# Kernel tuning notes

Measured on AMD Instinct MI355X. Metric: run time of the kernel, lower is better.

## Reference

```python
import jax, jax.numpy as jnp
import numpy as np

KS = 7                 # sconv_kernel_size
PAD = (KS - 1) // 2
SIMS_SCALE = 10.0      # sims_norm_scale
EPS = 1e-5


def setup_inputs() -> dict:
    key = jax.random.key(0)
    k1, k2, k3, k4 = jax.random.split(key, 4)
    T, C, H, W = 4, 3, 192, 192
    S = 300
    x = jax.random.normal(k1, (T, C, H, W), jnp.float32)
    spix = jax.random.randint(k2, (T, H, W), 0, S, dtype=jnp.int32)
    W_lin = jax.random.normal(k3, (C, C * KS * KS), jnp.float32) * 0.05
    b_lin = jax.random.normal(k4, (C,), jnp.float32) * 0.05
    return {"x": x, "spix": spix, "W_lin": W_lin, "b_lin": b_lin, "n_spix": S}


def _get_sims(x, spix, n_spix, scale):
    # x: [T,C,H,W], spix: [T,H,W] with contiguous ids in [0, n_spix)
    T, C, H, W = x.shape
    feats = x.transpose(0, 2, 3, 1).reshape(T, H * W, C)   # t (h w) f
    ids = spix.reshape(T, H * W)

    def pool(f, i):
        s = jax.ops.segment_sum(f, i, num_segments=n_spix)                      # [S,C]
        c = jax.ops.segment_sum(jnp.ones((f.shape[0],), f.dtype), i, num_segments=n_spix)  # [S]
        return s / jnp.maximum(c, 1.0)[:, None], c

    means, cnt = jax.vmap(pool)(feats, ids)                # [T,S,C], [T,S]
    # squared euclidean distance (cdist ** 2)
    d2 = (jnp.sum(feats * feats, -1)[:, :, None]
          + jnp.sum(means * means, -1)[:, None, :]
          - 2.0 * jnp.einsum('tnc,tsc->tns', feats, means))
    d2 = jnp.maximum(d2, 0.0)                              # [T,HW,S]
    # superpixels absent from frame t get distance inf (pwd[mask] = inf)
    d2 = jnp.where((cnt > 0)[:, None, :], d2, jnp.inf)
    sims = jax.nn.softmax(-scale * d2, axis=-1)            # softmax over superpixels
    return sims.reshape(T, H, W, n_spix)                   # [T,H,W,S]


def _prod_attn(sims):
    # non-local 'prod' search, zero flow, ws=KS: dot product of sims vectors
    # between each pixel and its KSxKS neighborhood (zero-padded borders)
    T, H, W, S = sims.shape
    p = jnp.pad(sims, ((0, 0), (PAD, PAD), (PAD, PAD), (0, 0)))
    attn = [jnp.einsum('thws,thws->thw', sims, p[:, dy:dy + H, dx:dx + W, :])
            for dy in range(KS) for dx in range(KS)]
    return jnp.stack(attn, -1)                             # [T,H,W,KS*KS]


def _unfold(x):
    # torch.nn.Unfold(kernel_size=KS, padding=PAD): zero pad, row-major window
    T, C, H, W = x.shape
    p = jnp.pad(x, ((0, 0), (0, 0), (PAD, PAD), (PAD, PAD)))
    pats = [p[:, :, dy:dy + H, dx:dx + W] for dy in range(KS) for dx in range(KS)]
    return jnp.stack(pats, 2)                              # [T,C,KS*KS,H,W]


def reference(x, spix, W_lin, b_lin, n_spix):
    T, C, H, W = x.shape
    sims = _get_sims(x, spix, n_spix, SIMS_SCALE)          # [T,H,W,S]
    rw = _prod_attn(sims)                                  # [T,H,W,K2]
    # apply_norm('max'): divide by max over neighborhood
    rw = rw / (EPS + jnp.max(rw, axis=-1, keepdims=True))
    Wk = W_lin.reshape(W_lin.shape[0], C, KS * KS)         # [od,id,k2]
    pats = _unfold(x)                                      # [T,id,k2,H,W]
    # out[t,o,h,w] = sum_{i,k} W[o,i,k] * rw[t,h,w,k] * patch[t,i,k,h,w] + b[o]
    out = jnp.einsum('oik,thwk,tikhw->tohw', Wk, rw, pats) + b_lin[None, :, None, None]
    return out
```

## Files before the change

kernel.cpp:

```cpp
#include <hip/hip_runtime.h>
#include <math.h>

#define TT 4
#define HH 192
#define WW 192
#define SS 300
#define SP 320
#define HW (HH*WW)
#define PD 3
#define HSZ 22
#define NHP 484
#define PSTRG 486
#define LOG2E 1.44269504088896340736f
#define NSEG 72
#define MEANS 360448
#define MOFF 393216
#define ZOFF (MOFF + TT*HW)

typedef _Float16 h8 __attribute__((ext_vector_type(8)));
typedef float f4 __attribute__((ext_vector_type(4)));


__launch_bounds__(256)
__global__ void k_accum(const float* __restrict__ x, const int* __restrict__ spix,
                        float* __restrict__ ws) {
    __shared__ float ls[SS * 4];
    const int tid = threadIdx.x;
    const int t = blockIdx.y, seg = blockIdx.x;
    for (int i = tid; i < SS * 4; i += 256) ls[i] = 0.f;
    __syncthreads();
    const int pb = seg * 512 + tid * 2;
#pragma unroll
    for (int it = 0; it < 2; it++) {
        int s = spix[t * HW + pb + it];
        atomicAdd(&ls[s * 4 + 0], x[(t * 3 + 0) * HW + pb + it]);
        atomicAdd(&ls[s * 4 + 1], x[(t * 3 + 1) * HW + pb + it]);
        atomicAdd(&ls[s * 4 + 2], x[(t * 3 + 2) * HW + pb + it]);
        atomicAdd(&ls[s * 4 + 3], 1.f);
    }
    __syncthreads();
    float* part = ws + (t * NSEG + seg) * 1200;
    for (int i = tid; i < SS * 4; i += 256) part[i] = ls[i];
}

__launch_bounds__(256)
__global__ void k_prep(const float* __restrict__ x, float* __restrict__ ws) {
    __shared__ float4 sm[SP];
    const int tid = threadIdx.x;
    const int t = blockIdx.y;
    const float* part = ws + t * NSEG * 1200;
    for (int i = tid; i < SP; i += 256) {
        float4 m;
        if (i < SS) {
            float s0 = 0.f, s1 = 0.f, s2 = 0.f, c = 0.f;
            for (int g = 0; g < NSEG; g++) {
                s0 += part[g * 1200 + i * 4 + 0];
                s1 += part[g * 1200 + i * 4 + 1];
                s2 += part[g * 1200 + i * 4 + 2];
                c  += part[g * 1200 + i * 4 + 3];
            }
            float inv = 1.f / fmaxf(c, 1.f);
            float mx = s0 * inv, my = s1 * inv, mz = s2 * inv;
            m.x = 20.f * LOG2E * mx; m.y = 20.f * LOG2E * my; m.z = 20.f * LOG2E * mz;
            m.w = (c > 0.f) ? (-10.f * LOG2E * (mx * mx + my * my + mz * mz)) : -INFINITY;
        } else {
            m.x = 0.f; m.y = 0.f; m.z = 0.f; m.w = -INFINITY;
        }
        sm[i] = m;
        if (blockIdx.x == 0) ((float4*)(ws + MEANS))[t * SP + i] = m;
    }
    __syncthreads();

    const int p0 = blockIdx.x * 512 + tid;
    const int p1 = p0 + 256;
    const float f0x = x[(t * 3 + 0) * HW + p0], f0y = x[(t * 3 + 1) * HW + p0], f0z = x[(t * 3 + 2) * HW + p0];
    const float f1x = x[(t * 3 + 0) * HW + p1], f1y = x[(t * 3 + 1) * HW + p1], f1z = x[(t * 3 + 2) * HW + p1];

    float M0 = -INFINITY, M1 = -INFINITY;
#pragma unroll 4
    for (int s = 0; s < SS; s++) {
        float4 a = sm[s];
        M0 = fmaxf(M0, fmaf(f0x, a.x, fmaf(f0y, a.y, fmaf(f0z, a.z, a.w))));
        M1 = fmaxf(M1, fmaf(f1x, a.x, fmaf(f1y, a.y, fmaf(f1z, a.z, a.w))));
    }
    float Z0 = 0.f, Z1 = 0.f;
#pragma unroll 4
    for (int s = 0; s < SS; s++) {
        float4 a = sm[s];
        Z0 += exp2f(fmaf(f0x, a.x, fmaf(f0y, a.y, fmaf(f0z, a.z, a.w))) - M0);
        Z1 += exp2f(fmaf(f1x, a.x, fmaf(f1y, a.y, fmaf(f1z, a.z, a.w))) - M1);
    }
    ws[MOFF + t * HW + p0] = M0;
    ws[MOFF + t * HW + p1] = M1;
    ws[ZOFF + t * HW + p0] = 1.f / Z0;
    ws[ZOFF + t * HW + p1] = 1.f / Z1;
}

#define REP49(M) M(0)M(1)M(2)M(3)M(4)M(5)M(6)M(7)M(8)M(9)M(10)M(11)M(12)M(13) \
    M(14)M(15)M(16)M(17)M(18)M(19)M(20)M(21)M(22)M(23)M(24)M(25)M(26)M(27) \
    M(28)M(29)M(30)M(31)M(32)M(33)M(34)M(35)M(36)M(37)M(38)M(39)M(40)M(41) \
    M(42)M(43)M(44)M(45)M(46)M(47)M(48)

#define QOFF(k) (((k) / 7 - PD) * HSZ + ((k) % 7 - PD))


__launch_bounds__(512, 2)
__global__ void k_main(const float* __restrict__ x, const float* __restrict__ Wlin,
                       const float* __restrict__ blin, const float* __restrict__ ws,
                       float* __restrict__ out) {
    __shared__ __align__(16) char ebuf[2][8 * PSTRG * 16];
    __shared__ float4 sfh[NHP];
    __shared__ float  sW[441];
    __shared__ float4 smean[SP];

    const int tid = threadIdx.x;
    const int wid = tid >> 6, lane = tid & 63;
    const int pxc = lane & 15, kg = lane >> 4;
    const int t = blockIdx.z;
    const int gx0 = blockIdx.x * 16 - PD, gy0 = blockIdx.y * 16 - PD;
    const float4* m4 = (const float4*)(ws + MEANS) + t * SP;

    for (int i = tid; i < 441; i += 512) sW[i] = Wlin[i];
    for (int i = tid; i < SP; i += 512) smean[i] = m4[i];

    float fx = 0.f, fy = 0.f, fz = 0.f, M = INFINITY;
    if (tid < NHP) {
        int hy = tid / HSZ, hx = tid - hy * HSZ;
        int gy = gy0 + hy, gx = gx0 + hx;
        float iZ = 0.f;
        if (gy >= 0 && gy < HH && gx >= 0 && gx < WW) {
            int p = gy * WW + gx;
            fx = x[(t * 3 + 0) * HW + p];
            fy = x[(t * 3 + 1) * HW + p];
            fz = x[(t * 3 + 2) * HW + p];
            M  = ws[MOFF + t * HW + p];
            iZ = ws[ZOFF + t * HW + p];
        }
        sfh[tid] = make_float4(fx, fy, fz, iZ);
    }
    __syncthreads();

#define PHASEB(cc, bb) if (tid < NHP) { \
        char* dst = ebuf[bb]; \
        _Pragma("unroll") \
        for (int jd = 0; jd < 8; jd++) { \
            h8 v; \
            _Pragma("unroll") \
            for (int e = 0; e < 4; e++) { \
                float4 ma = smean[(cc) * 64 + jd * 8 + 2 * e]; \
                float4 mb = smean[(cc) * 64 + jd * 8 + 2 * e + 1]; \
                float E0 = exp2f(fmaf(fx, ma.x, fmaf(fy, ma.y, fmaf(fz, ma.z, ma.w))) - M); \
                float E1 = exp2f(fmaf(fx, mb.x, fmaf(fy, mb.y, fmaf(fz, mb.z, mb.w))) - M); \
                auto pr = __builtin_amdgcn_cvt_pkrtz(E0, E1); \
                v[2 * e] = (_Float16)pr.x; v[2 * e + 1] = (_Float16)pr.y; \
            } \
            *(h8*)(dst + (jd * PSTRG + tid) * 16) = v; \
        } }

    const int r0 = 2 * wid;
    const int gA0 = kg * PSTRG + (r0 + PD) * HSZ + PD + pxc;
    const int gA1 = gA0 + HSZ;
    const int bcol2 = (16 + pxc > 21) ? 21 : 16 + pxc;
    const int gB1 = kg * PSTRG + r0 * HSZ + pxc;
    const int gB2 = kg * PSTRG + r0 * HSZ + bcol2;

    f4 zero4 = {0.f, 0.f, 0.f, 0.f};
    f4 aP[7], aQ[7], aR[7], aS[7];
#pragma unroll
    for (int d = 0; d < 7; d++) { aP[d] = zero4; aQ[d] = zero4; aR[d] = zero4; aS[d] = zero4; }

#define MFMA_STEP(pbk) { \
        h8 A0 = *(const h8*)((pbk) + gA0 * 16); \
        h8 A1 = *(const h8*)((pbk) + gA1 * 16); \
        h8 c1 = *(const h8*)((pbk) + gB1 * 16); \
        h8 c2 = *(const h8*)((pbk) + gB2 * 16); \
        h8 n1 = *(const h8*)((pbk) + (gB1 + HSZ) * 16); \
        h8 n2 = *(const h8*)((pbk) + (gB2 + HSZ) * 16); \
        aP[0] = __builtin_amdgcn_mfma_f32_16x16x32_f16(A0, c1, aP[0], 0, 0, 0); \
        aQ[0] = __builtin_amdgcn_mfma_f32_16x16x32_f16(A0, c2, aQ[0], 0, 0, 0); \
        _Pragma("unroll") \
        for (int d = 1; d < 7; d++) { \
            h8 f1 = *(const h8*)((pbk) + (gB1 + (d + 1) * HSZ) * 16); \
            h8 f2 = *(const h8*)((pbk) + (gB2 + (d + 1) * HSZ) * 16); \
            aP[d]     = __builtin_amdgcn_mfma_f32_16x16x32_f16(A0, n1, aP[d], 0, 0, 0); \
            aR[d - 1] = __builtin_amdgcn_mfma_f32_16x16x32_f16(A1, n1, aR[d - 1], 0, 0, 0); \
            aQ[d]     = __builtin_amdgcn_mfma_f32_16x16x32_f16(A0, n2, aQ[d], 0, 0, 0); \
            aS[d - 1] = __builtin_amdgcn_mfma_f32_16x16x32_f16(A1, n2, aS[d - 1], 0, 0, 0); \
            n1 = f1; n2 = f2; \
        } \
        aR[6] = __builtin_amdgcn_mfma_f32_16x16x32_f16(A1, n1, aR[6], 0, 0, 0); \
        aS[6] = __builtin_amdgcn_mfma_f32_16x16x32_f16(A1, n2, aS[6], 0, 0, 0); }

#define MFMA_CHUNK { \
        __builtin_amdgcn_s_setprio(1); \
        MFMA_STEP(pb) \
        MFMA_STEP(pb + 4 * PSTRG * 16) \
        __builtin_amdgcn_s_setprio(0); }

    PHASEB(0, 0)

#pragma unroll 1
    for (int c = 0; c < 5; c++) {
        __syncthreads();
        const char* pb = ebuf[c & 1];
        if (wid & 1) {
            MFMA_CHUNK
            if (c < 4) { PHASEB(c + 1, (c + 1) & 1) }
        } else {
            if (c < 4) { PHASEB(c + 1, (c + 1) & 1) }
            MFMA_CHUNK
        }
    }
    __syncthreads();

    float* attn = (float*)ebuf;
#pragma unroll
    for (int d = 0; d < 7; d++) {
#pragma unroll
        for (int reg = 0; reg < 4; reg++) {
            int i = 4 * kg + reg;
            int u1 = pxc - i;
            int u2 = u1 + 16;
            if ((unsigned)u1 <= 6u) {
                attn[(r0 * 16 + i) * 51 + d * 7 + u1] = aP[d][reg];
                attn[((r0 + 1) * 16 + i) * 51 + d * 7 + u1] = aR[d][reg];
            }
            if ((unsigned)u2 <= 6u) {
                attn[(r0 * 16 + i) * 51 + d * 7 + u2] = aQ[d][reg];
                attn[((r0 + 1) * 16 + i) * 51 + d * 7 + u2] = aS[d][reg];
            }
        }
    }
    __syncthreads();

    if (tid < 256) {
        const int r = tid >> 4, cq = tid & 15;
        const int own = (r + PD) * HSZ + (cq + PD);
        const float* ap = attn + tid * 51;
        float mx = 0.f;
#define PK1(k) mx = fmaxf(mx, ap[k] * sfh[own + QOFF(k)].w);
        REP49(PK1)
#undef PK1
        const float iZp = sfh[own].w;
        const float inv = 1.f / (1e-5f / iZp + mx);

        float o0 = blin[0], o1 = blin[1], o2 = blin[2];
#define PK2(k) { float4 f = sfh[own + QOFF(k)]; \
        float rwk = ap[k] * f.w * inv; \
        o0 += rwk * (sW[k] * f.x + sW[49 + (k)] * f.y + sW[98 + (k)] * f.z); \
        o1 += rwk * (sW[147 + (k)] * f.x + sW[196 + (k)] * f.y + sW[245 + (k)] * f.z); \
        o2 += rwk * (sW[294 + (k)] * f.x + sW[343 + (k)] * f.y + sW[392 + (k)] * f.z); }
        REP49(PK2)
#undef PK2

        int p = (gy0 + PD + r) * WW + gx0 + PD + cq;
        out[(t * 3 + 0) * HW + p] = o0;
        out[(t * 3 + 1) * HW + p] = o1;
        out[(t * 3 + 2) * HW + p] = o2;
    }
}

extern "C" void kernel_launch(void* const* d_in, const int* in_sizes, int n_in,
                              void* d_out, int out_size, void* d_ws, size_t ws_size,
                              hipStream_t stream) {
    (void)in_sizes; (void)n_in; (void)out_size; (void)ws_size;
    const float* x    = (const float*)d_in[0];
    const int*   spix = (const int*)d_in[1];
    const float* Wlin = (const float*)d_in[2];
    const float* blin = (const float*)d_in[3];
    float* out = (float*)d_out;
    float* ws  = (float*)d_ws;

    hipLaunchKernelGGL(k_accum, dim3(NSEG, TT), dim3(256), 0, stream, x, spix, ws);
    hipLaunchKernelGGL(k_prep,  dim3(HW / 512, TT), dim3(256), 0, stream, x, ws);
    hipLaunchKernelGGL(k_main,  dim3(WW / 16, HH / 16, TT), dim3(512), 0, stream,
                       x, Wlin, blin, ws, out);
}
```

Before: 131.3 us.

## Shrink main-kernel tile to 12x16 and switch exp2 to fast expf

```diff
diff --git a/kernel.cpp b/kernel.cpp
--- a/kernel.cpp
+++ b/kernel.cpp
@@ -8,10 +8,12 @@
 #define SP 320
 #define HW (HH*WW)
 #define PD 3
-#define HSZ 22
-#define NHP 484
-#define PSTRG 486
-#define LOG2E 1.44269504088896340736f
+#define TSW 12
+#define TSH 16
+#define HLW 18
+#define HLH 22
+#define NHP (HLH*HLW)
+#define PSTRG 400
 #define NSEG 72
 #define MEANS 360448
 #define MOFF 393216
@@ -61,8 +63,8 @@
             }
             float inv = 1.f / fmaxf(c, 1.f);
             float mx = s0 * inv, my = s1 * inv, mz = s2 * inv;
-            m.x = 20.f * LOG2E * mx; m.y = 20.f * LOG2E * my; m.z = 20.f * LOG2E * mz;
-            m.w = (c > 0.f) ? (-10.f * LOG2E * (mx * mx + my * my + mz * mz)) : -INFINITY;
+            m.x = 20.f * mx; m.y = 20.f * my; m.z = 20.f * mz;
+            m.w = (c > 0.f) ? (-10.f * (mx * mx + my * my + mz * mz)) : -INFINITY;
         } else {
             m.x = 0.f; m.y = 0.f; m.z = 0.f; m.w = -INFINITY;
         }
@@ -87,8 +89,8 @@
 #pragma unroll 4
     for (int s = 0; s < SS; s++) {
         float4 a = sm[s];
-        Z0 += exp2f(fmaf(f0x, a.x, fmaf(f0y, a.y, fmaf(f0z, a.z, a.w))) - M0);
-        Z1 += exp2f(fmaf(f1x, a.x, fmaf(f1y, a.y, fmaf(f1z, a.z, a.w))) - M1);
+        Z0 += __expf(fmaf(f0x, a.x, fmaf(f0y, a.y, fmaf(f0z, a.z, a.w))) - M0);
+        Z1 += __expf(fmaf(f1x, a.x, fmaf(f1y, a.y, fmaf(f1z, a.z, a.w))) - M1);
     }
     ws[MOFF + t * HW + p0] = M0;
     ws[MOFF + t * HW + p1] = M1;
@@ -101,7 +103,7 @@
     M(28)M(29)M(30)M(31)M(32)M(33)M(34)M(35)M(36)M(37)M(38)M(39)M(40)M(41) \
     M(42)M(43)M(44)M(45)M(46)M(47)M(48)
 
-#define QOFF(k) (((k) / 7 - PD) * HSZ + ((k) % 7 - PD))
+#define QOFF(k) (((k) / 7 - PD) * HLW + ((k) % 7 - PD))
 
 
 __launch_bounds__(512, 2)
@@ -117,7 +119,7 @@
     const int wid = tid >> 6, lane = tid & 63;
     const int pxc = lane & 15, kg = lane >> 4;
     const int t = blockIdx.z;
-    const int gx0 = blockIdx.x * 16 - PD, gy0 = blockIdx.y * 16 - PD;
+    const int gx0 = blockIdx.x * TSW - PD, gy0 = blockIdx.y * TSH - PD;
     const float4* m4 = (const float4*)(ws + MEANS) + t * SP;
 
     for (int i = tid; i < 441; i += 512) sW[i] = Wlin[i];
@@ -125,7 +127,7 @@
 
     float fx = 0.f, fy = 0.f, fz = 0.f, M = INFINITY;
     if (tid < NHP) {
-        int hy = tid / HSZ, hx = tid - hy * HSZ;
+        int hy = tid / HLW, hx = tid - hy * HLW;
         int gy = gy0 + hy, gx = gx0 + hx;
         float iZ = 0.f;
         if (gy >= 0 && gy < HH && gx >= 0 && gx < WW) {
@@ -149,8 +151,8 @@
             for (int e = 0; e < 4; e++) { \
                 float4 ma = smean[(cc) * 64 + jd * 8 + 2 * e]; \
                 float4 mb = smean[(cc) * 64 + jd * 8 + 2 * e + 1]; \
-                float E0 = exp2f(fmaf(fx, ma.x, fmaf(fy, ma.y, fmaf(fz, ma.z, ma.w))) - M); \
-                float E1 = exp2f(fmaf(fx, mb.x, fmaf(fy, mb.y, fmaf(fz, mb.z, mb.w))) - M); \
+                float E0 = __expf(fmaf(fx, ma.x, fmaf(fy, ma.y, fmaf(fz, ma.z, ma.w))) - M); \
+                float E1 = __expf(fmaf(fx, mb.x, fmaf(fy, mb.y, fmaf(fz, mb.z, mb.w))) - M); \
                 auto pr = __builtin_amdgcn_cvt_pkrtz(E0, E1); \
                 v[2 * e] = (_Float16)pr.x; v[2 * e + 1] = (_Float16)pr.y; \
             } \
@@ -158,11 +160,12 @@
         } }
 
     const int r0 = 2 * wid;
-    const int gA0 = kg * PSTRG + (r0 + PD) * HSZ + PD + pxc;
-    const int gA1 = gA0 + HSZ;
-    const int bcol2 = (16 + pxc > 21) ? 21 : 16 + pxc;
-    const int gB1 = kg * PSTRG + r0 * HSZ + pxc;
-    const int gB2 = kg * PSTRG + r0 * HSZ + bcol2;
+    const int acol = (pxc > 14) ? 14 : pxc;
+    const int gA0 = kg * PSTRG + (r0 + PD) * HLW + PD + acol;
+    const int gA1 = gA0 + HLW;
+    const int bcol2 = (16 + pxc > 17) ? 17 : 16 + pxc;
+    const int gB1 = kg * PSTRG + r0 * HLW + pxc;
+    const int gB2 = kg * PSTRG + r0 * HLW + bcol2;
 
     f4 zero4 = {0.f, 0.f, 0.f, 0.f};
     f4 aP[7], aQ[7], aR[7], aS[7];
@@ -174,14 +177,14 @@
         h8 A1 = *(const h8*)((pbk) + gA1 * 16); \
         h8 c1 = *(const h8*)((pbk) + gB1 * 16); \
         h8 c2 = *(const h8*)((pbk) + gB2 * 16); \
-        h8 n1 = *(const h8*)((pbk) + (gB1 + HSZ) * 16); \
-        h8 n2 = *(const h8*)((pbk) + (gB2 + HSZ) * 16); \
+        h8 n1 = *(const h8*)((pbk) + (gB1 + HLW) * 16); \
+        h8 n2 = *(const h8*)((pbk) + (gB2 + HLW) * 16); \
         aP[0] = __builtin_amdgcn_mfma_f32_16x16x32_f16(A0, c1, aP[0], 0, 0, 0); \
         aQ[0] = __builtin_amdgcn_mfma_f32_16x16x32_f16(A0, c2, aQ[0], 0, 0, 0); \
         _Pragma("unroll") \
         for (int d = 1; d < 7; d++) { \
-            h8 f1 = *(const h8*)((pbk) + (gB1 + (d + 1) * HSZ) * 16); \
-            h8 f2 = *(const h8*)((pbk) + (gB2 + (d + 1) * HSZ) * 16); \
+            h8 f1 = *(const h8*)((pbk) + (gB1 + (d + 1) * HLW) * 16); \
+            h8 f2 = *(const h8*)((pbk) + (gB2 + (d + 1) * HLW) * 16); \
             aP[d]     = __builtin_amdgcn_mfma_f32_16x16x32_f16(A0, n1, aP[d], 0, 0, 0); \
             aR[d - 1] = __builtin_amdgcn_mfma_f32_16x16x32_f16(A1, n1, aR[d - 1], 0, 0, 0); \
             aQ[d]     = __builtin_amdgcn_mfma_f32_16x16x32_f16(A0, n2, aQ[d], 0, 0, 0); \
@@ -221,21 +224,23 @@
             int i = 4 * kg + reg;
             int u1 = pxc - i;
             int u2 = u1 + 16;
-            if ((unsigned)u1 <= 6u) {
-                attn[(r0 * 16 + i) * 51 + d * 7 + u1] = aP[d][reg];
-                attn[((r0 + 1) * 16 + i) * 51 + d * 7 + u1] = aR[d][reg];
+            if (i < TSW) {
+                if ((unsigned)u1 <= 6u) {
+                    attn[(r0 * TSW + i) * 51 + d * 7 + u1] = aP[d][reg];
+                    attn[((r0 + 1) * TSW + i) * 51 + d * 7 + u1] = aR[d][reg];
+                }
+                if ((unsigned)u2 <= 6u) {
+                    attn[(r0 * TSW + i) * 51 + d * 7 + u2] = aQ[d][reg];
+                    attn[((r0 + 1) * TSW + i) * 51 + d * 7 + u2] = aS[d][reg];
+                }
             }
-            if ((unsigned)u2 <= 6u) {
-                attn[(r0 * 16 + i) * 51 + d * 7 + u2] = aQ[d][reg];
-                attn[((r0 + 1) * 16 + i) * 51 + d * 7 + u2] = aS[d][reg];
-            }
-        }
-    }
-    __syncthreads();
-
-    if (tid < 256) {
-        const int r = tid >> 4, cq = tid & 15;
-        const int own = (r + PD) * HSZ + (cq + PD);
+        }
+    }
+    __syncthreads();
+
+    if (tid < TSH * TSW) {
+        const int r = tid / TSW, cq = tid - r * TSW;
+        const int own = (r + PD) * HLW + (cq + PD);
         const float* ap = attn + tid * 51;
         float mx = 0.f;
 #define PK1(k) mx = fmaxf(mx, ap[k] * sfh[own + QOFF(k)].w);
@@ -273,6 +278,6 @@
 
     hipLaunchKernelGGL(k_accum, dim3(NSEG, TT), dim3(256), 0, stream, x, spix, ws);
     hipLaunchKernelGGL(k_prep,  dim3(HW / 512, TT), dim3(256), 0, stream, x, ws);
-    hipLaunchKernelGGL(k_main,  dim3(WW / 16, HH / 16, TT), dim3(512), 0, stream,
+    hipLaunchKernelGGL(k_main,  dim3(WW / TSW, HH / TSH, TT), dim3(512), 0, stream,
                        x, Wlin, blin, ws, out);
 }
```

After: 116.4 us. -11.4%, faster.
